# Kernel tuning notes

Measured on AMD Instinct MI355X. Metric: run time of the kernel, lower is better.

Reference implementation:

```python
import jax, jax.numpy as jnp
import numpy as np
import math

B, T, C, H = 4, 2048, 1024, 4
D = C // H
SCALE = 1.0 / math.sqrt(D)
EPS = 1e-5

def _cln(x, w, b):
    # channel-first LayerNorm over C of (B, C, T)
    mu = jnp.mean(x, axis=1, keepdims=True)
    r = x - mu
    s = jnp.mean(r * r, axis=1, keepdims=True)
    return r / jnp.sqrt(s + EPS) * w + b

def _dwconv(x, w, b=None):
    # depthwise conv1d: x (B, C, T), w (C, 1, 3), stride 1, pad 1
    y = jax.lax.conv_general_dilated(x, w, (1,), [(1, 1)], dimension_numbers=('NCH', 'OIH', 'NCH'), feature_group_count=x.shape[1])
    if b is not None:
        y = y + b[None, :, None]
    return y

def _conv1x1(x, w, b):
    # pointwise conv: x (B, C, T), w (Cout, Cin), b (Cout,)
    return jnp.einsum('oc,bct->bot', w, x) + b[None, :, None]

def _forward(x, mask, norm1_w, norm1_b, qconv_w, kconv_w, vconv_w, qnorm_w, qnorm_b, knorm_w, knorm_b, vnorm_w, vnorm_b, q1_w, q1_b, k1_w, k1_b, v1_w, v1_b, proj_w, proj_b, norm2_w, norm2_b, lin1_w, lin1_b, tc_w, tc_b, lin2_w, lin2_b):
    xc = jnp.swapaxes(x, 1, 2)                      # (B, C, T)
    h = _cln(xc, norm1_w, norm1_b)
    mf = mask.astype(x.dtype)                       # (B, 1, T); stride 1 -> interpolate is identity
    q = _conv1x1(_cln(_dwconv(h, qconv_w) * mf, qnorm_w, qnorm_b), q1_w, q1_b)
    k = _conv1x1(_cln(_dwconv(h, kconv_w) * mf, knorm_w, knorm_b), k1_w, k1_b)
    v = _conv1x1(_cln(_dwconv(h, vconv_w) * mf, vnorm_w, vnorm_b), v1_w, v1_b)
    # (B, H, T, D)
    q = jnp.swapaxes(q.reshape(B, H, D, T), 2, 3)
    k = jnp.swapaxes(k.reshape(B, H, D, T), 2, 3)
    v = jnp.swapaxes(v.reshape(B, H, D, T), 2, 3)
    att = jnp.einsum('bhqd,bhkd->bhqk', q * SCALE, k)
    att = jnp.where(mask[:, :, None, :], att, -jnp.inf)
    att = jax.nn.softmax(att, axis=-1)
    out = jnp.einsum('bhqk,bhkd->bhqd', att, v * mf[:, :, :, None])
    out = jnp.swapaxes(out, 2, 3).reshape(B, C, T)
    out = _conv1x1(out, proj_w, proj_b) * mf        # qx_mask == mask for stride 1
    x = x + jnp.swapaxes(out, 1, 2)                 # residual, (B, T, C)
    # Local_cnn branch
    h2 = jnp.swapaxes(_cln(jnp.swapaxes(x, 1, 2), norm2_w, norm2_b), 1, 2)  # (B, T, C)
    y = h2 @ lin1_w.T + lin1_b
    y = jnp.swapaxes(_dwconv(jnp.swapaxes(y, 1, 2), tc_w, tc_b), 1, 2)
    y = jax.nn.gelu(y, approximate=False)
    y = y @ lin2_w.T + lin2_b
    return x + y

def setup_inputs():
    key = jax.random.key(0)
    ks = jax.random.split(key, 16)
    f32 = jnp.float32
    x = jax.random.normal(ks[0], (B, T, C), dtype=f32)
    lengths = jax.random.randint(ks[1], (B,), T // 2, T + 1)
    mask = jnp.arange(T)[None, None, :] < lengths[:, None, None]  # (B, 1, T) bool
    dw_std = math.sqrt(2.0 / 3.0)
    px_std = math.sqrt(2.0 / C)
    d = dict(x=x, mask=mask)
    d['norm1_w'] = jnp.ones((1, C, 1), f32); d['norm1_b'] = jnp.zeros((1, C, 1), f32)
    d['qconv_w'] = jax.random.normal(ks[2], (C, 1, 3), dtype=f32) * dw_std
    d['kconv_w'] = jax.random.normal(ks[3], (C, 1, 3), dtype=f32) * dw_std
    d['vconv_w'] = jax.random.normal(ks[4], (C, 1, 3), dtype=f32) * dw_std
    for nm in ['qnorm', 'knorm', 'vnorm']:
        d[nm + '_w'] = jnp.ones((1, C, 1), f32); d[nm + '_b'] = jnp.zeros((1, C, 1), f32)
    d['q1_w'] = jax.random.normal(ks[5], (C, C), dtype=f32) * px_std; d['q1_b'] = jnp.zeros((C,), f32)
    d['k1_w'] = jax.random.normal(ks[6], (C, C), dtype=f32) * px_std; d['k1_b'] = jnp.zeros((C,), f32)
    d['v1_w'] = jax.random.normal(ks[7], (C, C), dtype=f32) * px_std; d['v1_b'] = jnp.zeros((C,), f32)
    d['proj_w'] = jax.random.normal(ks[8], (C, C), dtype=f32) * px_std; d['proj_b'] = jnp.zeros((C,), f32)
    d['norm2_w'] = jnp.ones((1, C, 1), f32); d['norm2_b'] = jnp.zeros((1, C, 1), f32)
    d['lin1_w'] = jax.random.normal(ks[9], (C, C), dtype=f32) * 0.02; d['lin1_b'] = jnp.zeros((C,), f32)
    d['tc_w'] = jax.random.normal(ks[10], (C, 1, 3), dtype=f32) * dw_std; d['tc_b'] = jnp.zeros((C,), f32)
    d['lin2_w'] = jax.random.normal(ks[11], (C, C), dtype=f32) * 0.02; d['lin2_b'] = jnp.zeros((C,), f32)
    return d

def reference(x, mask, norm1_w, norm1_b, qconv_w, kconv_w, vconv_w, qnorm_w, qnorm_b, knorm_w, knorm_b, vnorm_w, vnorm_b, q1_w, q1_b, k1_w, k1_b, v1_w, v1_b, proj_w, proj_b, norm2_w, norm2_b, lin1_w, lin1_b, tc_w, tc_b, lin2_w, lin2_b):
    return _forward(x, mask, norm1_w, norm1_b, qconv_w, kconv_w, vconv_w, qnorm_w, qnorm_b, knorm_w, knorm_b, vnorm_w, vnorm_b, q1_w, q1_b, k1_w, k1_b, v1_w, v1_b, proj_w, proj_b, norm2_w, norm2_b, lin1_w, lin1_b, tc_w, tc_b, lin2_w, lin2_b)
```

## Files before the change

kernel.cpp:

```cpp
#include <hip/hip_runtime.h>

#define BB 4
#define TT 2048
#define CC 1024
#define HH 4
#define DD 256
#define MM (BB*TT)

#define EPSV 1e-5f
#define NEGBIG (-1e30f)
#define SCALEV 0.0625f

typedef unsigned short u16;
typedef unsigned int   u32;
typedef __bf16 bf16x8 __attribute__((ext_vector_type(8)));
typedef float  f32x4  __attribute__((ext_vector_type(4)));

typedef u32 __attribute__((address_space(1))) gu32;
typedef u32 __attribute__((address_space(3))) lu32;

__device__ __forceinline__ u16 f2bf(float f){
  u32 u = __builtin_bit_cast(u32, f);
  u32 r = (u + 0x7fffu + ((u >> 16) & 1u)) >> 16;
  return (u16)r;
}
__device__ __forceinline__ float bf2f(u16 h){
  u32 u = ((u32)h) << 16;
  return __builtin_bit_cast(float, u);
}
__device__ __forceinline__ void gload_lds16(const u16* g, u16* l){
  __builtin_amdgcn_global_load_lds((const gu32*)g, (lu32*)l, 16, 0, 0);
}
__device__ __forceinline__ u32 cvtpk_bf16(float lo, float hi){
  u32 r;
  asm("v_cvt_pk_bf16_f32 %0, %1, %2" : "=v"(r) : "v"(lo), "v"(hi));
  return r;
}

__global__ __launch_bounds__(256) void conv_w_kernel(
    const float* __restrict__ w0, const float* __restrict__ w1, const float* __restrict__ w2,
    const float* __restrict__ w3, const float* __restrict__ w4, const float* __restrict__ w5,
    u16* __restrict__ o0, u16* __restrict__ o1, u16* __restrict__ o2,
    u16* __restrict__ o3, u16* __restrict__ o4, u16* __restrict__ o5){
  const int i = (blockIdx.x * 256 + threadIdx.x) * 4;
  const float* wsrc[6] = {w0,w1,w2,w3,w4,w5};
  u16* odst[6] = {o0,o1,o2,o3,o4,o5};
#pragma unroll
  for (int k = 0; k < 6; ++k){
    float4 v = *(const float4*)(wsrc[k] + i);
    ushort4 p; p.x=f2bf(v.x); p.y=f2bf(v.y); p.z=f2bf(v.z); p.w=f2bf(v.w);
    *(ushort4*)(odst[k] + i) = p;
  }
}

template<int OUTBF>
__global__ __launch_bounds__(256) void ln_rows(const float* __restrict__ x,
    const float* __restrict__ g, const float* __restrict__ be, void* __restrict__ out){
  const int row = blockIdx.x, tid = threadIdx.x;
  const float4 v = ((const float4*)(x + (size_t)row * CC))[tid];
  float s  = v.x + v.y + v.z + v.w;
  float ss = v.x*v.x + v.y*v.y + v.z*v.z + v.w*v.w;
  __shared__ float sb[8];
#pragma unroll
  for (int o = 1; o < 64; o <<= 1){ s += __shfl_xor(s, o); ss += __shfl_xor(ss, o); }
  const int wid = tid >> 6, lane = tid & 63;
  if (lane == 0){ sb[wid] = s; sb[4 + wid] = ss; }
  __syncthreads();
  s  = sb[0] + sb[1] + sb[2] + sb[3];
  ss = sb[4] + sb[5] + sb[6] + sb[7];
  const float mu = s * (1.0f / CC);
  const float rstd = rsqrtf(ss * (1.0f / CC) - mu * mu + EPSV);
  const float4 gg = ((const float4*)g)[tid];
  const float4 bb = ((const float4*)be)[tid];
  const float r0 = (v.x - mu) * rstd * gg.x + bb.x;
  const float r1 = (v.y - mu) * rstd * gg.y + bb.y;
  const float r2 = (v.z - mu) * rstd * gg.z + bb.z;
  const float r3 = (v.w - mu) * rstd * gg.w + bb.w;
  if (OUTBF){
    ushort4 p; p.x=f2bf(r0); p.y=f2bf(r1); p.z=f2bf(r2); p.w=f2bf(r3);
    *(ushort4*)((u16*)out + (size_t)row * CC + tid * 4) = p;
  } else {
    ((float4*)((float*)out + (size_t)row * CC))[tid] = make_float4(r0, r1, r2, r3);
  }
}

__global__ __launch_bounds__(256) void qkv_pre(const float* __restrict__ h,
    const int* __restrict__ mask,
    const float* __restrict__ qw, const float* __restrict__ kw, const float* __restrict__ vw,
    const float* __restrict__ qg, const float* __restrict__ qb2,
    const float* __restrict__ kg, const float* __restrict__ kb2,
    const float* __restrict__ vg, const float* __restrict__ vb2,
    u16* __restrict__ qn, u16* __restrict__ kn, u16* __restrict__ vn){
  const int row = blockIdx.x, tid = threadIdx.x;
  const int t = row & (TT - 1);
  const float mf = mask[row] ? 1.f : 0.f;
  const float4 z4 = make_float4(0.f, 0.f, 0.f, 0.f);
  const float4 x0 = ((const float4*)(h + (size_t)row * CC))[tid];
  const float4 xm = (t > 0)      ? ((const float4*)(h + (size_t)(row - 1) * CC))[tid] : z4;
  const float4 xp = (t < TT - 1) ? ((const float4*)(h + (size_t)(row + 1) * CC))[tid] : z4;
  const int c = tid * 4;
  const float am[4] = {xm.x, xm.y, xm.z, xm.w};
  const float a0[4] = {x0.x, x0.y, x0.z, x0.w};
  const float ap[4] = {xp.x, xp.y, xp.z, xp.w};
  float yq[4], yk[4], yv[4];
  float sq=0.f, ssq=0.f, sk=0.f, ssk=0.f, sv=0.f, ssv=0.f;
#pragma unroll
  for (int i = 0; i < 4; ++i){
    const float* qwp = qw + (c + i) * 3;
    const float* kwp = kw + (c + i) * 3;
    const float* vwp = vw + (c + i) * 3;
    const float q_ = (am[i]*qwp[0] + a0[i]*qwp[1] + ap[i]*qwp[2]) * mf;
    const float k_ = (am[i]*kwp[0] + a0[i]*kwp[1] + ap[i]*kwp[2]) * mf;
    const float v_ = (am[i]*vwp[0] + a0[i]*vwp[1] + ap[i]*vwp[2]) * mf;
    yq[i]=q_; yk[i]=k_; yv[i]=v_;
    sq+=q_; ssq+=q_*q_; sk+=k_; ssk+=k_*k_; sv+=v_; ssv+=v_*v_;
  }
  __shared__ float sb[24];
#pragma unroll
  for (int o = 1; o < 64; o <<= 1){
    sq += __shfl_xor(sq, o); ssq += __shfl_xor(ssq, o);
    sk += __shfl_xor(sk, o); ssk += __shfl_xor(ssk, o);
    sv += __shfl_xor(sv, o); ssv += __shfl_xor(ssv, o);
  }
  const int wid = tid >> 6, lane = tid & 63;
  if (lane == 0){
    sb[wid]=sq; sb[4+wid]=ssq; sb[8+wid]=sk; sb[12+wid]=ssk; sb[16+wid]=sv; sb[20+wid]=ssv;
  }
  __syncthreads();
  sq  = sb[0]+sb[1]+sb[2]+sb[3];    ssq = sb[4]+sb[5]+sb[6]+sb[7];
  sk  = sb[8]+sb[9]+sb[10]+sb[11];  ssk = sb[12]+sb[13]+sb[14]+sb[15];
  sv  = sb[16]+sb[17]+sb[18]+sb[19];ssv = sb[20]+sb[21]+sb[22]+sb[23];
  {
    const float mu = sq * (1.f/CC), rstd = rsqrtf(ssq*(1.f/CC) - mu*mu + EPSV);
    ushort4 p;
    p.x = f2bf((yq[0]-mu)*rstd*qg[c+0] + qb2[c+0]);
    p.y = f2bf((yq[1]-mu)*rstd*qg[c+1] + qb2[c+1]);
    p.z = f2bf((yq[2]-mu)*rstd*qg[c+2] + qb2[c+2]);
    p.w = f2bf((yq[3]-mu)*rstd*qg[c+3] + qb2[c+3]);
    *(ushort4*)(qn + (size_t)row * CC + c) = p;
  }
  {
    const float mu = sk * (1.f/CC), rstd = rsqrtf(ssk*(1.f/CC) - mu*mu + EPSV);
    ushort4 p;
    p.x = f2bf((yk[0]-mu)*rstd*kg[c+0] + kb2[c+0]);
    p.y = f2bf((yk[1]-mu)*rstd*kg[c+1] + kb2[c+1]);
    p.z = f2bf((yk[2]-mu)*rstd*kg[c+2] + kb2[c+2]);
    p.w = f2bf((yk[3]-mu)*rstd*kg[c+3] + kb2[c+3]);
    *(ushort4*)(kn + (size_t)row * CC + c) = p;
  }
  {
    const float mu = sv * (1.f/CC), rstd = rsqrtf(ssv*(1.f/CC) - mu*mu + EPSV);
    ushort4 p;
    p.x = f2bf((yv[0]-mu)*rstd*vg[c+0] + vb2[c+0]);
    p.y = f2bf((yv[1]-mu)*rstd*vg[c+1] + vb2[c+1]);
    p.z = f2bf((yv[2]-mu)*rstd*vg[c+2] + vb2[c+2]);
    p.w = f2bf((yv[3]-mu)*rstd*vg[c+3] + vb2[c+3]);
    *(ushort4*)(vn + (size_t)row * CC + c) = p;
  }
}

template<int MODE>
__global__ __launch_bounds__(256) void gemm_bt(
    const u16* __restrict__ A, const u16* __restrict__ Bw,
    const float* __restrict__ bias, void* __restrict__ out,
    const float* __restrict__ resid, const int* __restrict__ mask){
  __shared__ u16 As[128 * 32];
  __shared__ u16 Bs[128 * 32];
  const int tid = threadIdx.x, lane = tid & 63, wid = tid >> 6;
  const int wr = wid >> 1, wc = wid & 1;
  const int bm = blockIdx.x, bn = blockIdx.y;
  f32x4 acc[4][4];
#pragma unroll
  for (int i = 0; i < 4; ++i)
#pragma unroll
    for (int j = 0; j < 4; ++j) acc[i][j] = (f32x4){0.f, 0.f, 0.f, 0.f};
  const u16* gA = A  + (size_t)(bm * 128 + wid * 32 + (lane >> 2)) * CC + (lane & 3) * 8;
  const u16* gB = Bw + (size_t)(bn * 128 + wid * 32 + (lane >> 2)) * CC + (lane & 3) * 8;
  u16* lA = &As[wid * 1024];
  u16* lB = &Bs[wid * 1024];
  const int la = lane & 15, lg8 = (lane >> 4) * 8;
  for (int kt = 0; kt < CC / 32; ++kt){
    gload_lds16(gA + kt * 32, lA);
    gload_lds16(gA + kt * 32 + (size_t)16 * CC, lA + 512);
    gload_lds16(gB + kt * 32, lB);
    gload_lds16(gB + kt * 32 + (size_t)16 * CC, lB + 512);
    __syncthreads();
    bf16x8 af[4], bf[4];
#pragma unroll
    for (int mi = 0; mi < 4; ++mi) af[mi] = *(const bf16x8*)&As[(wr*64 + mi*16 + la)*32 + lg8];
#pragma unroll
    for (int ni = 0; ni < 4; ++ni) bf[ni] = *(const bf16x8*)&Bs[(wc*64 + ni*16 + la)*32 + lg8];
#pragma unroll
    for (int mi = 0; mi < 4; ++mi)
#pragma unroll
      for (int ni = 0; ni < 4; ++ni)
        acc[mi][ni] = __builtin_amdgcn_mfma_f32_16x16x32_bf16(af[mi], bf[ni], acc[mi][ni], 0, 0, 0);
    __syncthreads();
  }
  const int lg = lane >> 4;
#pragma unroll
  for (int mi = 0; mi < 4; ++mi){
    const int mb = bm * 128 + wr * 64 + mi * 16 + lg * 4;
#pragma unroll
    for (int ni = 0; ni < 4; ++ni){
      const int n = bn * 128 + wc * 64 + ni * 16 + la;
      const float bz = bias[n];
      if (MODE == 0){
        u16* o = (u16*)out;
#pragma unroll
        for (int j = 0; j < 4; ++j) o[(size_t)(mb + j) * CC + n] = f2bf(acc[mi][ni][j] + bz);
      } else if (MODE == 1){
        float* o = (float*)out;
#pragma unroll
        for (int j = 0; j < 4; ++j){
          const int m = mb + j;
          const float mf = mask[m] ? 1.f : 0.f;
          o[(size_t)m * CC + n] = (acc[mi][ni][j] + bz) * mf + resid[(size_t)m * CC + n];
        }
      } else if (MODE == 2){
        float* o = (float*)out;
#pragma unroll
        for (int j = 0; j < 4; ++j){
          const int m = mb + j;
          o[(size_t)m * CC + n] = acc[mi][ni][j] + bz + resid[(size_t)m * CC + n];
        }
      } else {
        u16* o = (u16*)out;
        const int bq = mb >> 11, tq = mb & (TT - 1);
        const int hq = n >> 8, dq = n & 255;
        ushort4 p;
        p.x = f2bf(acc[mi][ni][0] + bz); p.y = f2bf(acc[mi][ni][1] + bz);
        p.z = f2bf(acc[mi][ni][2] + bz); p.w = f2bf(acc[mi][ni][3] + bz);
        *(ushort4*)&o[(size_t)((bq * HH + hq) * DD + dq) * TT + tq] = p;
      }
    }
  }
}

__global__ __launch_bounds__(256, 2) void flash_attn(
    const u16* __restrict__ Q, const u16* __restrict__ Kg,
    const u16* __restrict__ Vt, const int* __restrict__ mask,
    u16* __restrict__ Oa){
  __shared__ __align__(16) u16 Ks[2][32 * 256];
  __shared__ __align__(16) u16 Vs[2][1280 * 8];
  __shared__ __align__(16) u16 Ps[4][640];
  const int Dn = blockIdx.x;
  const int bh = (Dn & 7) * 2 + ((Dn >> 3) >> 5);
  const int qt = (Dn >> 3) & 31;
  const int b = bh >> 2, h2 = bh & 3;
  const int tid = threadIdx.x, lane = tid & 63, wid = tid >> 6;
  const int la = lane & 15, lg = lane >> 4;

  const int* mrow = mask + b * TT;
  int len = 1024;
  {
    unsigned long long bal = __ballot(mrow[1024 + lane * 16] != 0);
    int ones = __popcll(bal);
    if (ones > 0){
      int lo = 1024 + (ones - 1) * 16;
      unsigned long long bal2 = __ballot(mrow[lo + la] != 0);
      len = lo + __popcll(bal2 & 0xFFFFull);
    }
  }
  const int nkt = (len + 31) >> 5;

  bf16x8 qf[8];
  const u16* qrow = Q + (size_t)(b * TT + qt * 64 + wid * 16 + la) * CC + h2 * DD + lg * 8;
#pragma unroll
  for (int kd = 0; kd < 8; ++kd) qf[kd] = *(const bf16x8*)(qrow + kd * 32);

  f32x4 oacc[16];
#pragma unroll
  for (int i = 0; i < 16; ++i) oacc[i] = (f32x4){0.f, 0.f, 0.f, 0.f};
  float mrun = NEGBIG, lrun = 0.f;

  const int krow = tid >> 5, kchk = tid & 31;
  const u16* ksrc = Kg + (size_t)(b * TT + krow) * CC + h2 * DD + (kchk ^ (krow & 7)) * 8;
  u16* KsW = &Ks[0][0];
  u16* VsW = &Vs[0][0];

  auto stageK = [&](int KT, int BUF){
#pragma unroll
    for (int i = 0; i < 4; ++i)
      gload_lds16(ksrc + (size_t)(KT * 32 + i * 8) * CC,
                  KsW + BUF * 8192 + i * 2048 + wid * 512);
  };
  auto stageV = [&](int KT, int BUF){
#pragma unroll
    for (int i = 0; i < 5; ++i){
      const int g = i * 256 + tid;
      const int dd = g / 5, cc = g % 5;
      if (cc < 4)
        gload_lds16(Vt + (size_t)(bh * DD + dd) * TT + KT * 32 + cc * 8,
                    VsW + BUF * 10240 + i * 2048 + wid * 512);
    }
  };

  stageK(0, 0); stageV(0, 0);
  __syncthreads();

  char* PsB = (char*)&Ps[wid][0];
  const int swk = (la & 7) << 4;
  const float sc2 = SCALEV * 1.44269504f;

  for (int kt = 0; kt < nkt; ++kt){
    const int cur = kt & 1;
    if (kt + 1 < nkt){ stageK(kt + 1, cur ^ 1); stageV(kt + 1, cur ^ 1); }
    const char* KsB = (const char*)&Ks[cur][0];
    const char* VsB = (const char*)&Vs[cur][0];
    f32x4 sfr[2];
#pragma unroll
    for (int fn = 0; fn < 2; ++fn){
      f32x4 s = (f32x4){0.f, 0.f, 0.f, 0.f};
      const int rk = fn * 16 + la;
#pragma unroll
      for (int kd = 0; kd < 8; ++kd){
        bf16x8 kf = *(const bf16x8*)(KsB + rk * 512 + ((kd * 64 + lg * 16) ^ swk));
        s = __builtin_amdgcn_mfma_f32_16x16x32_bf16(kf, qf[kd], s, 0, 0, 0);
      }
      sfr[fn] = s;
    }
    if (kt * 32 + 32 <= len){
      sfr[0] *= sc2; sfr[1] *= sc2;
    } else {
      const int kb = kt * 32 + lg * 4;
#pragma unroll
      for (int fn = 0; fn < 2; ++fn)
#pragma unroll
        for (int j = 0; j < 4; ++j)
          sfr[fn][j] = (kb + fn * 16 + j < len) ? sfr[fn][j] * sc2 : NEGBIG;
    }
    float tm = fmaxf(fmaxf(fmaxf(sfr[0][0], sfr[0][1]), fmaxf(sfr[0][2], sfr[0][3])),
                     fmaxf(fmaxf(sfr[1][0], sfr[1][1]), fmaxf(sfr[1][2], sfr[1][3])));
    tm = fmaxf(tm, __shfl_xor(tm, 16));
    tm = fmaxf(tm, __shfl_xor(tm, 32));
    if (!__all(tm <= mrun + 12.0f)){
      const float mn = fmaxf(mrun, tm);
      const float al = __builtin_exp2f(mrun - mn);
      mrun = mn; lrun *= al;
#pragma unroll
      for (int i = 0; i < 16; ++i) oacc[i] *= al;
    }
    float p0 = __builtin_exp2f(sfr[0][0] - mrun), p1 = __builtin_exp2f(sfr[0][1] - mrun);
    float p2 = __builtin_exp2f(sfr[0][2] - mrun), p3 = __builtin_exp2f(sfr[0][3] - mrun);
    float p4 = __builtin_exp2f(sfr[1][0] - mrun), p5 = __builtin_exp2f(sfr[1][1] - mrun);
    float p6 = __builtin_exp2f(sfr[1][2] - mrun), p7 = __builtin_exp2f(sfr[1][3] - mrun);
    float ts = ((p0 + p1) + (p2 + p3)) + ((p4 + p5) + (p6 + p7));
    ts += __shfl_xor(ts, 16);
    ts += __shfl_xor(ts, 32);
    lrun += ts;
    {
      uint2 w0; w0.x = cvtpk_bf16(p0, p1); w0.y = cvtpk_bf16(p2, p3);
      uint2 w1; w1.x = cvtpk_bf16(p4, p5); w1.y = cvtpk_bf16(p6, p7);
      *(uint2*)(PsB + la * 80 + lg * 8) = w0;
      *(uint2*)(PsB + la * 80 + 32 + lg * 8) = w1;
    }
    bf16x8 pf = *(const bf16x8*)(PsB + la * 80 + lg * 16);
#pragma unroll
    for (int mi = 0; mi < 16; ++mi){
      bf16x8 vf = *(const bf16x8*)(VsB + (mi * 16 + la) * 80 + lg * 16);
      oacc[mi] = __builtin_amdgcn_mfma_f32_16x16x32_bf16(vf, pf, oacc[mi], 0, 0, 0);
    }
    __syncthreads();
  }
  const float inv = 1.f / lrun;
  u16* orow = Oa + (size_t)(b * TT + qt * 64 + wid * 16 + la) * CC + h2 * DD + lg * 4;
#pragma unroll
  for (int mi = 0; mi < 16; ++mi){
    ushort4 p;
    p.x = f2bf(oacc[mi][0] * inv); p.y = f2bf(oacc[mi][1] * inv);
    p.z = f2bf(oacc[mi][2] * inv); p.w = f2bf(oacc[mi][3] * inv);
    *(ushort4*)(orow + mi * 16) = p;
  }
}

__global__ __launch_bounds__(256) void tc_gelu(const u16* __restrict__ y2,
    const float* __restrict__ w, const float* __restrict__ bias, u16* __restrict__ y3){
  const int row = blockIdx.x, tid = threadIdx.x;
  const int t = row & (TT - 1);
  const int c = tid * 4;
  ushort4 z4; z4.x = z4.y = z4.z = z4.w = 0;
  const ushort4 u0 = *(const ushort4*)(y2 + (size_t)row * CC + c);
  const ushort4 um = (t > 0)      ? *(const ushort4*)(y2 + (size_t)(row - 1) * CC + c) : z4;
  const ushort4 up = (t < TT - 1) ? *(const ushort4*)(y2 + (size_t)(row + 1) * CC + c) : z4;
  const float am[4] = {bf2f(um.x), bf2f(um.y), bf2f(um.z), bf2f(um.w)};
  const float a0[4] = {bf2f(u0.x), bf2f(u0.y), bf2f(u0.z), bf2f(u0.w)};
  const float ap[4] = {bf2f(up.x), bf2f(up.y), bf2f(up.z), bf2f(up.w)};
  u16 pv[4];
#pragma unroll
  for (int i = 0; i < 4; ++i){
    const float* wp = w + (c + i) * 3;
    const float yv = am[i] * wp[0] + a0[i] * wp[1] + ap[i] * wp[2] + bias[c + i];
    const float ge = 0.5f * yv * (1.f + erff(yv * 0.7071067811865475f));
    pv[i] = f2bf(ge);
  }
  ushort4 p; p.x = pv[0]; p.y = pv[1]; p.z = pv[2]; p.w = pv[3];
  *(ushort4*)(y3 + (size_t)row * CC + c) = p;
}

extern "C" void kernel_launch(void* const* d_in, const int* in_sizes, int n_in,
                              void* d_out, int out_size, void* d_ws, size_t ws_size,
                              hipStream_t stream){
  const float* x     = (const float*)d_in[0];
  const int*   mask  = (const int*)d_in[1];
  const float* n1g   = (const float*)d_in[2];
  const float* n1b   = (const float*)d_in[3];
  const float* qconv = (const float*)d_in[4];
  const float* kconv = (const float*)d_in[5];
  const float* vconv = (const float*)d_in[6];
  const float* qg    = (const float*)d_in[7];
  const float* qbe   = (const float*)d_in[8];
  const float* kg    = (const float*)d_in[9];
  const float* kbe   = (const float*)d_in[10];
  const float* vg    = (const float*)d_in[11];
  const float* vbe   = (const float*)d_in[12];
  const float* q1w   = (const float*)d_in[13];
  const float* q1b   = (const float*)d_in[14];
  const float* k1w   = (const float*)d_in[15];
  const float* k1b   = (const float*)d_in[16];
  const float* v1w   = (const float*)d_in[17];
  const float* v1b   = (const float*)d_in[18];
  const float* pw    = (const float*)d_in[19];
  const float* pb    = (const float*)d_in[20];
  const float* n2g   = (const float*)d_in[21];
  const float* n2b   = (const float*)d_in[22];
  const float* l1w   = (const float*)d_in[23];
  const float* l1b   = (const float*)d_in[24];
  const float* tcw   = (const float*)d_in[25];
  const float* tcb   = (const float*)d_in[26];
  const float* l2w   = (const float*)d_in[27];
  const float* l2b   = (const float*)d_in[28];
  (void)in_sizes; (void)n_in; (void)out_size; (void)ws_size;

  char* ws = (char*)d_ws;
  const size_t MB = (size_t)1 << 20;
  u16* wq  = (u16*)(ws + 0 * MB);
  u16* wk  = (u16*)(ws + 2 * MB);
  u16* wv  = (u16*)(ws + 4 * MB);
  u16* wp2 = (u16*)(ws + 6 * MB);
  u16* wl1 = (u16*)(ws + 8 * MB);
  u16* wl2 = (u16*)(ws + 10 * MB);
  float* hbuf = (float*)(ws + 12 * MB);
  float* x2   = hbuf;
  u16* qn  = (u16*)(ws + 44 * MB);
  u16* kn  = (u16*)(ws + 60 * MB);
  u16* vn  = (u16*)(ws + 76 * MB);
  u16* Qb  = (u16*)(ws + 92 * MB);
  u16* Kb  = (u16*)(ws + 108 * MB);
  u16* Vtb = (u16*)(ws + 124 * MB);
  u16* AO  = qn;
  u16* y1  = kn;
  u16* y2  = vn;
  u16* y3  = Qb;

  conv_w_kernel<<<1024, 256, 0, stream>>>(q1w, k1w, v1w, pw, l1w, l2w, wq, wk, wv, wp2, wl1, wl2);
  ln_rows<0><<<MM, 256, 0, stream>>>(x, n1g, n1b, hbuf);
  qkv_pre<<<MM, 256, 0, stream>>>(hbuf, mask, qconv, kconv, vconv,
                                  qg, qbe, kg, kbe, vg, vbe, qn, kn, vn);
  gemm_bt<0><<<dim3(64, 8), 256, 0, stream>>>(qn, wq, q1b, Qb, nullptr, nullptr);
  gemm_bt<0><<<dim3(64, 8), 256, 0, stream>>>(kn, wk, k1b, Kb, nullptr, nullptr);
  gemm_bt<3><<<dim3(64, 8), 256, 0, stream>>>(vn, wv, v1b, Vtb, nullptr, nullptr);
  flash_attn<<<512, 256, 0, stream>>>(Qb, Kb, Vtb, mask, AO);
  gemm_bt<1><<<dim3(64, 8), 256, 0, stream>>>(AO, wp2, pb, x2, x, mask);
  ln_rows<1><<<MM, 256, 0, stream>>>(x2, n2g, n2b, y1);
  gemm_bt<0><<<dim3(64, 8), 256, 0, stream>>>(y1, wl1, l1b, y2, nullptr, nullptr);
  tc_gelu<<<MM, 256, 0, stream>>>(y2, tcw, tcb, y3);
  gemm_bt<2><<<dim3(64, 8), 256, 0, stream>>>(y3, wl2, l2b, (float*)d_out, x2, nullptr);
}
```

Before: 376.5 us.

## Double flash-attention query tile per wave and swizzle V/P shared layouts

Each wave now handles 32 query rows instead of 16, so every K and V fragment read from shared memory feeds two MFMAs, and the grid shrinks from 512 to 256 blocks. The padded 80-byte V and P row layouts are replaced by 64-byte rows with an XOR swizzle, which removes the predicated fifth load in V staging and is meant to avoid bank conflicts. The trade-off is twice the accumulator registers, since the occupancy hint of 2 is dropped. Halving the block count may also leave compute units underused on a 256-CU part.

```diff
diff --git a/kernel.cpp b/kernel.cpp
--- a/kernel.cpp
+++ b/kernel.cpp
@@ -237,16 +237,16 @@
   }
 }
 
-__global__ __launch_bounds__(256, 2) void flash_attn(
+__global__ __launch_bounds__(256) void flash_attn(
     const u16* __restrict__ Q, const u16* __restrict__ Kg,
     const u16* __restrict__ Vt, const int* __restrict__ mask,
     u16* __restrict__ Oa){
-  __shared__ __align__(16) u16 Ks[2][32 * 256];
-  __shared__ __align__(16) u16 Vs[2][1280 * 8];
-  __shared__ __align__(16) u16 Ps[4][640];
+  __shared__ __align__(16) u16 Ks[2][8192];
+  __shared__ __align__(16) u16 Vs[2][8192];
+  __shared__ __align__(16) u16 Ps[4][1024];
   const int Dn = blockIdx.x;
-  const int bh = (Dn & 7) * 2 + ((Dn >> 3) >> 5);
-  const int qt = (Dn >> 3) & 31;
+  const int xcd = Dn & 7, idx = Dn >> 3;
+  const int bh = xcd * 2 + (idx >> 4), qt = idx & 15;
   const int b = bh >> 2, h2 = bh & 3;
   const int tid = threadIdx.x, lane = tid & 63, wid = tid >> 6;
   const int la = lane & 15, lg = lane >> 4;
@@ -264,18 +264,25 @@
   }
   const int nkt = (len + 31) >> 5;
 
-  bf16x8 qf[8];
-  const u16* qrow = Q + (size_t)(b * TT + qt * 64 + wid * 16 + la) * CC + h2 * DD + lg * 8;
-#pragma unroll
-  for (int kd = 0; kd < 8; ++kd) qf[kd] = *(const bf16x8*)(qrow + kd * 32);
-
-  f32x4 oacc[16];
-#pragma unroll
-  for (int i = 0; i < 16; ++i) oacc[i] = (f32x4){0.f, 0.f, 0.f, 0.f};
-  float mrun = NEGBIG, lrun = 0.f;
+  bf16x8 qf[8][2];
+#pragma unroll
+  for (int qn2 = 0; qn2 < 2; ++qn2){
+    const u16* qrow = Q + (size_t)(b * TT + qt * 128 + wid * 32 + qn2 * 16 + la) * CC
+                      + h2 * DD + lg * 8;
+#pragma unroll
+    for (int kd = 0; kd < 8; ++kd) qf[kd][qn2] = *(const bf16x8*)(qrow + kd * 32);
+  }
+
+  f32x4 oacc[16][2];
+#pragma unroll
+  for (int i = 0; i < 16; ++i){ oacc[i][0] = (f32x4){0,0,0,0}; oacc[i][1] = (f32x4){0,0,0,0}; }
+  float mrun[2] = {NEGBIG, NEGBIG}, lrun[2] = {0.f, 0.f};
 
   const int krow = tid >> 5, kchk = tid & 31;
   const u16* ksrc = Kg + (size_t)(b * TT + krow) * CC + h2 * DD + (kchk ^ (krow & 7)) * 8;
+  const int vdd = lane >> 2, vc = lane & 3;
+  const int vsw = (vc ^ ((vdd >> 1) & 3)) * 8;
+  const u16* vsrcb = Vt + (size_t)bh * DD * TT;
   u16* KsW = &Ks[0][0];
   u16* VsW = &Vs[0][0];
 
@@ -287,13 +294,9 @@
   };
   auto stageV = [&](int KT, int BUF){
 #pragma unroll
-    for (int i = 0; i < 5; ++i){
-      const int g = i * 256 + tid;
-      const int dd = g / 5, cc = g % 5;
-      if (cc < 4)
-        gload_lds16(Vt + (size_t)(bh * DD + dd) * TT + KT * 32 + cc * 8,
-                    VsW + BUF * 10240 + i * 2048 + wid * 512);
-    }
+    for (int i = 0; i < 4; ++i)
+      gload_lds16(vsrcb + (size_t)(i * 64 + wid * 16 + vdd) * TT + KT * 32 + vsw,
+                  VsW + BUF * 8192 + i * 2048 + wid * 512);
   };
 
   stageK(0, 0); stageV(0, 0);
@@ -301,6 +304,7 @@
 
   char* PsB = (char*)&Ps[wid][0];
   const int swk = (la & 7) << 4;
+  const int swv = (la >> 1) & 3;
   const float sc2 = SCALEV * 1.44269504f;
 
   for (int kt = 0; kt < nkt; ++kt){
@@ -308,69 +312,85 @@
     if (kt + 1 < nkt){ stageK(kt + 1, cur ^ 1); stageV(kt + 1, cur ^ 1); }
     const char* KsB = (const char*)&Ks[cur][0];
     const char* VsB = (const char*)&Vs[cur][0];
-    f32x4 sfr[2];
-#pragma unroll
-    for (int fn = 0; fn < 2; ++fn){
-      f32x4 s = (f32x4){0.f, 0.f, 0.f, 0.f};
-      const int rk = fn * 16 + la;
-#pragma unroll
-      for (int kd = 0; kd < 8; ++kd){
-        bf16x8 kf = *(const bf16x8*)(KsB + rk * 512 + ((kd * 64 + lg * 16) ^ swk));
-        s = __builtin_amdgcn_mfma_f32_16x16x32_bf16(kf, qf[kd], s, 0, 0, 0);
-      }
-      sfr[fn] = s;
+    f32x4 sfq[2][2];
+    sfq[0][0]=(f32x4){0,0,0,0}; sfq[0][1]=(f32x4){0,0,0,0};
+    sfq[1][0]=(f32x4){0,0,0,0}; sfq[1][1]=(f32x4){0,0,0,0};
+#pragma unroll
+    for (int kd = 0; kd < 8; ++kd){
+      const int co = (kd * 64 + lg * 16) ^ swk;
+      bf16x8 kf0 = *(const bf16x8*)(KsB + la * 512 + co);
+      bf16x8 kf1 = *(const bf16x8*)(KsB + (16 + la) * 512 + co);
+      sfq[0][0] = __builtin_amdgcn_mfma_f32_16x16x32_bf16(kf0, qf[kd][0], sfq[0][0], 0, 0, 0);
+      sfq[1][0] = __builtin_amdgcn_mfma_f32_16x16x32_bf16(kf0, qf[kd][1], sfq[1][0], 0, 0, 0);
+      sfq[0][1] = __builtin_amdgcn_mfma_f32_16x16x32_bf16(kf1, qf[kd][0], sfq[0][1], 0, 0, 0);
+      sfq[1][1] = __builtin_amdgcn_mfma_f32_16x16x32_bf16(kf1, qf[kd][1], sfq[1][1], 0, 0, 0);
     }
     if (kt * 32 + 32 <= len){
-      sfr[0] *= sc2; sfr[1] *= sc2;
+#pragma unroll
+      for (int qn2 = 0; qn2 < 2; ++qn2){ sfq[qn2][0] *= sc2; sfq[qn2][1] *= sc2; }
     } else {
       const int kb = kt * 32 + lg * 4;
 #pragma unroll
-      for (int fn = 0; fn < 2; ++fn)
-#pragma unroll
-        for (int j = 0; j < 4; ++j)
-          sfr[fn][j] = (kb + fn * 16 + j < len) ? sfr[fn][j] * sc2 : NEGBIG;
-    }
-    float tm = fmaxf(fmaxf(fmaxf(sfr[0][0], sfr[0][1]), fmaxf(sfr[0][2], sfr[0][3])),
-                     fmaxf(fmaxf(sfr[1][0], sfr[1][1]), fmaxf(sfr[1][2], sfr[1][3])));
-    tm = fmaxf(tm, __shfl_xor(tm, 16));
-    tm = fmaxf(tm, __shfl_xor(tm, 32));
-    if (!__all(tm <= mrun + 12.0f)){
-      const float mn = fmaxf(mrun, tm);
-      const float al = __builtin_exp2f(mrun - mn);
-      mrun = mn; lrun *= al;
-#pragma unroll
-      for (int i = 0; i < 16; ++i) oacc[i] *= al;
-    }
-    float p0 = __builtin_exp2f(sfr[0][0] - mrun), p1 = __builtin_exp2f(sfr[0][1] - mrun);
-    float p2 = __builtin_exp2f(sfr[0][2] - mrun), p3 = __builtin_exp2f(sfr[0][3] - mrun);
-    float p4 = __builtin_exp2f(sfr[1][0] - mrun), p5 = __builtin_exp2f(sfr[1][1] - mrun);
-    float p6 = __builtin_exp2f(sfr[1][2] - mrun), p7 = __builtin_exp2f(sfr[1][3] - mrun);
-    float ts = ((p0 + p1) + (p2 + p3)) + ((p4 + p5) + (p6 + p7));
-    ts += __shfl_xor(ts, 16);
-    ts += __shfl_xor(ts, 32);
-    lrun += ts;
-    {
+      for (int qn2 = 0; qn2 < 2; ++qn2)
+#pragma unroll
+        for (int fn = 0; fn < 2; ++fn)
+#pragma unroll
+          for (int j = 0; j < 4; ++j)
+            sfq[qn2][fn][j] = (kb + fn * 16 + j < len) ? sfq[qn2][fn][j] * sc2 : NEGBIG;
+    }
+    bf16x8 pf[2];
+#pragma unroll
+    for (int qn2 = 0; qn2 < 2; ++qn2){
+      float tm = fmaxf(fmaxf(fmaxf(sfq[qn2][0][0], sfq[qn2][0][1]),
+                             fmaxf(sfq[qn2][0][2], sfq[qn2][0][3])),
+                       fmaxf(fmaxf(sfq[qn2][1][0], sfq[qn2][1][1]),
+                             fmaxf(sfq[qn2][1][2], sfq[qn2][1][3])));
+      tm = fmaxf(tm, __shfl_xor(tm, 16));
+      tm = fmaxf(tm, __shfl_xor(tm, 32));
+      if (!__all(tm <= mrun[qn2] + 12.0f)){
+        const float mn = fmaxf(mrun[qn2], tm);
+        const float al = __builtin_exp2f(mrun[qn2] - mn);
+        mrun[qn2] = mn; lrun[qn2] *= al;
+#pragma unroll
+        for (int i = 0; i < 16; ++i) oacc[i][qn2] *= al;
+      }
+      const float m0 = mrun[qn2];
+      float p0 = __builtin_exp2f(sfq[qn2][0][0] - m0), p1 = __builtin_exp2f(sfq[qn2][0][1] - m0);
+      float p2 = __builtin_exp2f(sfq[qn2][0][2] - m0), p3 = __builtin_exp2f(sfq[qn2][0][3] - m0);
+      float p4 = __builtin_exp2f(sfq[qn2][1][0] - m0), p5 = __builtin_exp2f(sfq[qn2][1][1] - m0);
+      float p6 = __builtin_exp2f(sfq[qn2][1][2] - m0), p7 = __builtin_exp2f(sfq[qn2][1][3] - m0);
+      float ts = ((p0 + p1) + (p2 + p3)) + ((p4 + p5) + (p6 + p7));
+      ts += __shfl_xor(ts, 16);
+      ts += __shfl_xor(ts, 32);
+      lrun[qn2] += ts;
       uint2 w0; w0.x = cvtpk_bf16(p0, p1); w0.y = cvtpk_bf16(p2, p3);
       uint2 w1; w1.x = cvtpk_bf16(p4, p5); w1.y = cvtpk_bf16(p6, p7);
-      *(uint2*)(PsB + la * 80 + lg * 8) = w0;
-      *(uint2*)(PsB + la * 80 + 32 + lg * 8) = w1;
-    }
-    bf16x8 pf = *(const bf16x8*)(PsB + la * 80 + lg * 16);
+      char* pr = PsB + (qn2 * 16 + la) * 64 + ((lg & 1) << 3);
+      *(uint2*)(pr + ((((lg >> 1)    ) ^ swv) << 4)) = w0;
+      *(uint2*)(pr + (((2 + (lg >> 1)) ^ swv) << 4)) = w1;
+    }
+    pf[0] = *(const bf16x8*)(PsB + la * 64 + ((lg ^ swv) << 4));
+    pf[1] = *(const bf16x8*)(PsB + (16 + la) * 64 + ((lg ^ swv) << 4));
 #pragma unroll
     for (int mi = 0; mi < 16; ++mi){
-      bf16x8 vf = *(const bf16x8*)(VsB + (mi * 16 + la) * 80 + lg * 16);
-      oacc[mi] = __builtin_amdgcn_mfma_f32_16x16x32_bf16(vf, pf, oacc[mi], 0, 0, 0);
+      bf16x8 vf = *(const bf16x8*)(VsB + (mi * 16 + la) * 64 + ((lg ^ swv) << 4));
+      oacc[mi][0] = __builtin_amdgcn_mfma_f32_16x16x32_bf16(vf, pf[0], oacc[mi][0], 0, 0, 0);
+      oacc[mi][1] = __builtin_amdgcn_mfma_f32_16x16x32_bf16(vf, pf[1], oacc[mi][1], 0, 0, 0);
     }
     __syncthreads();
   }
-  const float inv = 1.f / lrun;
-  u16* orow = Oa + (size_t)(b * TT + qt * 64 + wid * 16 + la) * CC + h2 * DD + lg * 4;
-#pragma unroll
-  for (int mi = 0; mi < 16; ++mi){
-    ushort4 p;
-    p.x = f2bf(oacc[mi][0] * inv); p.y = f2bf(oacc[mi][1] * inv);
-    p.z = f2bf(oacc[mi][2] * inv); p.w = f2bf(oacc[mi][3] * inv);
-    *(ushort4*)(orow + mi * 16) = p;
+#pragma unroll
+  for (int qn2 = 0; qn2 < 2; ++qn2){
+    const float inv = 1.f / lrun[qn2];
+    u16* orow = Oa + (size_t)(b * TT + qt * 128 + wid * 32 + qn2 * 16 + la) * CC
+                + h2 * DD + lg * 4;
+#pragma unroll
+    for (int mi = 0; mi < 16; ++mi){
+      ushort4 p;
+      p.x = f2bf(oacc[mi][qn2][0] * inv); p.y = f2bf(oacc[mi][qn2][1] * inv);
+      p.z = f2bf(oacc[mi][qn2][2] * inv); p.w = f2bf(oacc[mi][qn2][3] * inv);
+      *(ushort4*)(orow + mi * 16) = p;
+    }
   }
 }
 
@@ -460,7 +480,7 @@
   gemm_bt<0><<<dim3(64, 8), 256, 0, stream>>>(qn, wq, q1b, Qb, nullptr, nullptr);
   gemm_bt<0><<<dim3(64, 8), 256, 0, stream>>>(kn, wk, k1b, Kb, nullptr, nullptr);
   gemm_bt<3><<<dim3(64, 8), 256, 0, stream>>>(vn, wv, v1b, Vtb, nullptr, nullptr);
-  flash_attn<<<512, 256, 0, stream>>>(Qb, Kb, Vtb, mask, AO);
+  flash_attn<<<256, 256, 0, stream>>>(Qb, Kb, Vtb, mask, AO);
   gemm_bt<1><<<dim3(64, 8), 256, 0, stream>>>(AO, wp2, pb, x2, x, mask);
   ln_rows<1><<<MM, 256, 0, stream>>>(x2, n2g, n2b, y1);
   gemm_bt<0><<<dim3(64, 8), 256, 0, stream>>>(y1, wl1, l1b, y2, nullptr, nullptr);
```

Measured after the change: 419.2 us. 1.11x slower.
